# Kernel tuning notes

Measured on AMD Instinct MI355X. Metric: run time of the kernel, lower is better.

Reference implementation:

```python
import jax, jax.numpy as jnp
import numpy as np

S, B, CIN, COUT, H, W, K = 4, 32, 128, 256, 16, 16, 3
D = CIN * K * K  # 1152, patch feature size = in_features
PRIOR_PREC = 1.0  # isotropic prior precision (prior_prec_full = PRIOR_PREC * I_D)
LOG_PREC_LR = 1.0


def _patches(x, k):
    # x: [N, C, H, W] -> [N, C*k*k, H, W]; channel-major patch ordering (matches torch unfold)
    pad = k // 2
    return jax.lax.conv_general_dilated_patches(
        x, (k, k), (1, 1), ((pad, pad), (pad, pad)),
        dimension_numbers=('NCHW', 'OIHW', 'NCHW'))


def setup_inputs() -> dict:
    key = jax.random.key(0)
    k1, k2, k3, k4 = jax.random.split(key, 4)
    X = jax.random.normal(k1, (S, B, CIN, H, W), jnp.float32)
    u = jax.random.normal(k2, (B, COUT, H, W), jnp.float32)
    log_prec_scaled = jax.random.normal(k3, (B,), jnp.float32)
    Z = jax.random.normal(k4, (S, COUT, D), jnp.float32)  # standard normal noise for rsample
    return {"X": X, "u": u, "log_prec_scaled": log_prec_scaled, "Z": Z}


def reference(X, u, log_prec_scaled, Z):
    Xi = X[:, :B]  # [S, B, CIN, H, W]
    sqrt_prec = jnp.exp(0.5 * LOG_PREC_LR * log_prec_scaled)[:, None, None, None]  # [B,1,1,1]
    Xil = sqrt_prec * Xi                     # [S, B, CIN, H, W]
    Yil = sqrt_prec * u                      # [B, COUT, H, W]

    # conv_mm: sufficient statistics via patch extraction
    P = _patches(Xil.reshape(S * B, CIN, H, W), K).reshape(S, B, D, H * W)
    Yf = Yil.reshape(B, COUT, H * W)
    XLX = jnp.einsum('sbdp,sbep->sde', P, P)       # [S, D, D]
    XLY = jnp.einsum('sbdp,bcp->sdc', P, Yf)       # [S, D, COUT]

    # rsample_logpq_weights
    prec = XLX + PRIOR_PREC * jnp.eye(D, dtype=XLX.dtype)   # [S, D, D]
    L = jnp.linalg.cholesky(prec)                            # [S, D, D], lower
    logdet_prec = 2.0 * jnp.sum(jnp.log(jnp.diagonal(L, axis1=-2, axis2=-1)), -1)  # [S]

    mu = jax.scipy.linalg.cho_solve((L, True), XLY)          # [S, D, COUT]
    # dW: solve L^T dW = Z (multi-RHS; L is shared across COUT)
    dW = jax.scipy.linalg.solve_triangular(L, jnp.swapaxes(Z, -1, -2), lower=True, trans='T')
    Wm = jnp.swapaxes(mu + dW, -1, -2)                       # [S, COUT, D]

    # logP: unnormalized MVN log-prob of each output neuron's weights under N(0, PRIOR_PREC^-1 I)
    logP = (0.5 * COUT * D * jnp.log(jnp.asarray(PRIOR_PREC, Wm.dtype))
            - 0.5 * PRIOR_PREC * jnp.sum(Wm * Wm, (-1, -2)))          # [S]
    logQ = -0.5 * jnp.sum(Z * Z, (-1, -2)) + 0.5 * COUT * logdet_prec  # [S]
    logpq = logP - logQ
    return Wm, logpq
```

## Files before the change

### kernel.cpp

```cpp
#include <hip/hip_runtime.h>
#include <math.h>

#define NS 4
#define NB 32
#define CIN 128
#define NCOUT 256
#define HWN 256
#define ND 1152
#define NK 8192
static const size_t D2 = (size_t)ND * ND;

typedef __attribute__((ext_vector_type(8))) short bf16x8;
typedef __attribute__((ext_vector_type(4))) float f32x4;

static __device__ inline unsigned short f2bf(float x) {
  unsigned int u = __float_as_uint(x);
  unsigned int r = (u + 0x7fffu + ((u >> 16) & 1u)) >> 16;
  return (unsigned short)r;
}
static __device__ inline float bf2f(unsigned short h) {
  return __uint_as_float(((unsigned int)h) << 16);
}
static __device__ inline float rdlane(float v, int l) {
  return __int_as_float(__builtin_amdgcn_readlane(__float_as_int(v), l));
}
static __device__ __forceinline__ void waitflag(const int* f) {
  while (__hip_atomic_load(f, __ATOMIC_RELAXED, __HIP_MEMORY_SCOPE_AGENT) == 0)
    __builtin_amdgcn_s_sleep(1);
  (void)__hip_atomic_load(f, __ATOMIC_ACQUIRE, __HIP_MEMORY_SCOPE_AGENT);
}


__global__ void k_sqrtp(const float* __restrict__ lp, float* __restrict__ sp,
                        float* __restrict__ pp) {
  int b = threadIdx.x;
  if (b < NB) sp[b] = expf(0.5f * lp[b]);
  if (b < 8) pp[b] = 0.f;
}

__global__ __launch_bounds__(128) void k_patches(const float* __restrict__ X,
                                                 const float* __restrict__ sp,
                                                 unsigned short* __restrict__ Phi,
                                                 unsigned short* __restrict__ Plo) {
  int d = blockIdx.x, s = blockIdx.y, t = threadIdx.x;
  int c = d / 9, r = d % 9, ky = r / 3, kx = r % 3;
  int p0 = t * 2;
  int yy = (p0 >> 4) + ky - 1;
  int xx0 = (p0 & 15) + kx - 1;
  bool oky = (yy >= 0 && yy < 16);
  bool ok0 = oky && (xx0 >= 0) && (xx0 < 16);
  bool ok1 = oky && (xx0 + 1 >= 0) && (xx0 + 1 < 16);
  int xo = yy * 16 + xx0;
  size_t base = ((size_t)s * ND + d) * NK + p0;
  for (int b = 0; b < NB; ++b) {
    float sb = sp[b];
    const float* xb = X + ((size_t)(s * NB + b) * CIN + c) * HWN;
    float v0 = ok0 ? xb[xo] * sb : 0.f;
    float v1 = ok1 ? xb[xo + 1] * sb : 0.f;
    unsigned short h0 = f2bf(v0), h1 = f2bf(v1);
    unsigned short l0 = f2bf(v0 - bf2f(h0)), l1 = f2bf(v1 - bf2f(h1));
    size_t idx = base + (size_t)b * HWN;
    *(unsigned int*)(Phi + idx) = (unsigned int)h0 | ((unsigned int)h1 << 16);
    *(unsigned int*)(Plo + idx) = (unsigned int)l0 | ((unsigned int)l1 << 16);
  }
}

__global__ __launch_bounds__(128) void k_ytt(const float* __restrict__ u,
                                             const float* __restrict__ sp,
                                             unsigned short* __restrict__ Yhi,
                                             unsigned short* __restrict__ Ylo) {
  int c = blockIdx.x, t = threadIdx.x;
  int p0 = t * 2;
  for (int b = 0; b < NB; ++b) {
    float sb = sp[b];
    const float* ub = u + ((size_t)b * NCOUT + c) * HWN + p0;
    float v0 = ub[0] * sb, v1 = ub[1] * sb;
    unsigned short h0 = f2bf(v0), h1 = f2bf(v1);
    unsigned short l0 = f2bf(v0 - bf2f(h0)), l1 = f2bf(v1 - bf2f(h1));
    size_t idx = (size_t)c * NK + (size_t)b * HWN + p0;
    *(unsigned int*)(Yhi + idx) = (unsigned int)h0 | ((unsigned int)h1 << 16);
    *(unsigned int*)(Ylo + idx) = (unsigned int)l0 | ((unsigned int)l1 << 16);
  }
}

__global__ __launch_bounds__(256) void k_gemm_mfma(
    const unsigned short* __restrict__ Phi, const unsigned short* __restrict__ Plo,
    const unsigned short* __restrict__ Yhi, const unsigned short* __restrict__ Ylo,
    float* __restrict__ prec, float* __restrict__ prec2,
    float* __restrict__ XLY, float* __restrict__ XLY2) {
  int jt = blockIdx.x, it = blockIdx.y;
  int s = blockIdx.z >> 1, kp = blockIdx.z & 1;
  bool isX = (jt <= it);
  if (!isX && jt < 9) return;
  int i0 = it * 128;
  int j0;
  const unsigned short *Bh, *Bl;
  if (isX) {
    j0 = jt * 128;
    Bh = Phi + ((size_t)s * ND + j0) * NK;
    Bl = Plo + ((size_t)s * ND + j0) * NK;
  } else {
    j0 = (jt - 9) * 128;
    Bh = Yhi + (size_t)j0 * NK;
    Bl = Ylo + (size_t)j0 * NK;
  }
  const unsigned short* Ah = Phi + ((size_t)s * ND + i0) * NK;
  const unsigned short* Al = Plo + ((size_t)s * ND + i0) * NK;

  __shared__ unsigned short sAh[4096], sAl[4096], sBh[4096], sBl[4096];
  int tid = threadIdx.x, wave = tid >> 6, lane = tid & 63;
  int wr = wave >> 1, wc = wave & 1;

  f32x4 zero = {0.f, 0.f, 0.f, 0.f};
  f32x4 acc[4][4];
#pragma unroll
  for (int m = 0; m < 4; ++m)
#pragma unroll
    for (int n = 0; n < 4; ++n) acc[m][n] = zero;

  const unsigned short* srcs[4] = {Ah, Al, Bh, Bl};
  unsigned short* dsts[4] = {sAh, sAl, sBh, sBl};
  int r0l = lane >> 2;
  int ke = (lane & 3) * 8;
  int arow0 = wr * 64 + (lane & 15);
  int brow0 = wc * 64 + (lane & 15);
  int koff = (lane >> 4) * 8;

  int kbeg = kp * (NK / 2), kend = kbeg + NK / 2;
  for (int k0 = kbeg; k0 < kend; k0 += 32) {
    __syncthreads();
#pragma unroll
    for (int f = 0; f < 4; ++f) {
#pragma unroll
      for (int cc = 0; cc < 2; ++cc) {
        int c = wave * 2 + cc;
        const unsigned short* g = srcs[f] + (size_t)(c * 16 + r0l) * NK + k0 + ke;
        unsigned short* l = dsts[f] + c * 512;
        __builtin_amdgcn_global_load_lds(
            (const __attribute__((address_space(1))) void*)g,
            (__attribute__((address_space(3))) void*)l, 16, 0, 0);
      }
    }
    __syncthreads();
    bf16x8 ah[4], al[4], bh[4], bl[4];
#pragma unroll
    for (int m = 0; m < 4; ++m) {
      int off = (arow0 + m * 16) * 32 + koff;
      ah[m] = *(const bf16x8*)&sAh[off];
      al[m] = *(const bf16x8*)&sAl[off];
    }
#pragma unroll
    for (int n = 0; n < 4; ++n) {
      int off = (brow0 + n * 16) * 32 + koff;
      bh[n] = *(const bf16x8*)&sBh[off];
      bl[n] = *(const bf16x8*)&sBl[off];
    }
#pragma unroll
    for (int m = 0; m < 4; ++m)
#pragma unroll
      for (int n = 0; n < 4; ++n) {
        acc[m][n] = __builtin_amdgcn_mfma_f32_16x16x32_bf16(ah[m], bh[n], acc[m][n], 0, 0, 0);
        acc[m][n] = __builtin_amdgcn_mfma_f32_16x16x32_bf16(ah[m], bl[n], acc[m][n], 0, 0, 0);
        acc[m][n] = __builtin_amdgcn_mfma_f32_16x16x32_bf16(al[m], bh[n], acc[m][n], 0, 0, 0);
      }
  }

  if (isX) {
    float* base = (kp ? prec2 : prec) + (size_t)s * D2;
#pragma unroll
    for (int m = 0; m < 4; ++m) {
      int row = i0 + wr * 64 + m * 16 + (lane >> 4) * 4;
#pragma unroll
      for (int n = 0; n < 4; ++n) {
        int col = j0 + wc * 64 + n * 16 + (lane & 15);
        float* cp = base + (size_t)row * ND + col;
#pragma unroll
        for (int r = 0; r < 4; ++r) cp[(size_t)r * ND] = acc[m][n][r];
      }
    }
  } else {
    float* base = (kp ? XLY2 : XLY) + (size_t)s * ND * NCOUT;
#pragma unroll
    for (int m = 0; m < 4; ++m) {
      int row = i0 + wr * 64 + m * 16 + (lane >> 4) * 4;
#pragma unroll
      for (int n = 0; n < 4; ++n) {
        int col = j0 + wc * 64 + n * 16 + (lane & 15);
        float* cp = base + (size_t)row * NCOUT + col;
#pragma unroll
        for (int r = 0; r < 4; ++r) cp[(size_t)r * NCOUT] = acc[m][n][r];
      }
    }
  }
}


static __device__ __forceinline__ void factor64(
    float acc[4][4], float (&At)[64][68], float (&Bt)[64][68],
    int tid, int lane, int w, int tx, int ty,
    float* iA64q, float* logdq, int* flagq) {
  __syncthreads();
#pragma unroll
  for (int r = 0; r < 4; ++r)
#pragma unroll
    for (int e = 0; e < 4; ++e) At[ty * 4 + r][tx * 4 + e] = acc[r][e];
  {
    int rr = tid >> 2, cb2 = (tid & 3) * 16;
#pragma unroll
    for (int m = 0; m < 16; ++m) Bt[rr][cb2 + m] = (rr == cb2 + m) ? 1.f : 0.f;
  }
  __syncthreads();
  float diagv = 1.f;
  for (int p = 0; p < 8; ++p) {
    int c0 = p * 8;
    if (w == 0) {
      float pa[8], xb[8];
#pragma unroll
      for (int e = 0; e < 8; ++e) {
        pa[e] = At[lane][c0 + e];
        xb[e] = Bt[c0 + e][lane];
      }
#pragma unroll
      for (int j = 0; j < 8; ++j) {
        float dj = rdlane(pa[j], c0 + j);
        float r0 = __builtin_amdgcn_rsqf(dj);
        r0 = r0 * (1.5f - 0.5f * dj * r0 * r0);
        pa[j] *= r0;
        float xj = xb[j] * r0;
        xb[j] = xj;
        if (lane == c0 + j) diagv = dj * r0;
#pragma unroll
        for (int e = j + 1; e < 8; ++e) {
          float sv = rdlane(pa[j], c0 + e);
          pa[e] = fmaf(-pa[j], sv, pa[e]);
          xb[e] = fmaf(-sv, xj, xb[e]);
        }
      }
#pragma unroll
      for (int e = 0; e < 8; ++e) {
        At[lane][c0 + e] = pa[e];
        Bt[c0 + e][lane] = xb[e];
      }
    }
    __syncthreads();
    if (p < 7) {
      float La[8], Xp[8];
#pragma unroll
      for (int e = 0; e < 8; ++e) {
        La[e] = At[lane][c0 + e];
        Xp[e] = Bt[c0 + e][lane];
      }
      for (int c = c0 + 8 + w; c < 64; c += 4) {
        float Lc[8];
#pragma unroll
        for (int e = 0; e < 8; ++e) Lc[e] = At[c][c0 + e];
        float v = At[lane][c], vb = Bt[c][lane];
#pragma unroll
        for (int e = 0; e < 8; ++e) {
          v = fmaf(-La[e], Lc[e], v);
          vb = fmaf(-Lc[e], Xp[e], vb);
        }
        At[lane][c] = v;
        Bt[c][lane] = vb;
      }
      __syncthreads();
    }
  }
  if (w == 0) logdq[lane] = logf(diagv);
  {
    float* q = iA64q;
    int rr = tid >> 2, cb2 = (tid & 3) * 16;
#pragma unroll
    for (int m = 0; m < 4; ++m)
      *(float4*)(q + rr * 64 + cb2 + m * 4) = *(const float4*)&Bt[rr][cb2 + m * 4];
  }
  __threadfence();
  __syncthreads();
  if (tid == 0)
    __hip_atomic_store(flagq, 1, __ATOMIC_RELEASE, __HIP_MEMORY_SCOPE_AGENT);
}

__global__ __launch_bounds__(256, 3) void k_chol_dag(
    float* __restrict__ L, const float* __restrict__ Lp2,
    float* __restrict__ iA64, float* __restrict__ logd,
    int* __restrict__ flags) {
  int t0 = blockIdx.x, s = blockIdx.y;
  int bi = 0;
  while ((bi + 1) * (bi + 2) / 2 <= t0) ++bi;
  int bj = t0 - bi * (bi + 1) / 2;
  int ib = bi * 64, jb = bj * 64;
  float* Ls = L + (size_t)s * D2;
  const float* Ps = Lp2 + (size_t)s * D2;
  int* fc = flags + s * 324;
  int* pd = flags + 1584 + s * 18;

  __shared__ float At[64][68];
  __shared__ float Bt[64][68];
  int tid = threadIdx.x, tx = tid & 15, ty = tid >> 4;
  int lane = tid & 63, w = tid >> 6;

  float acc[4][4];
#pragma unroll
  for (int r = 0; r < 4; ++r) {
    size_t idx = (size_t)(ib + ty * 4 + r) * ND + jb + tx * 4;
    float4 v = *(const float4*)(Ls + idx);
    float4 v2 = *(const float4*)(Ps + idx);
    acc[r][0] = v.x + v2.x; acc[r][1] = v.y + v2.y;
    acc[r][2] = v.z + v2.z; acc[r][3] = v.w + v2.w;
  }
  if (bi == bj) {
#pragma unroll
    for (int r = 0; r < 4; ++r)
#pragma unroll
      for (int e = 0; e < 4; ++e)
        if (ty * 4 + r == tx * 4 + e) acc[r][e] += 1.f;
  }

  int kend_t = (bi == bj) ? (bi > 0 ? bi - 1 : 0) : bj;
  for (int k = 0; k < kend_t; ++k) {
    waitflag(&fc[bi * 18 + k]);
    waitflag(&fc[bj * 18 + k]);
    int kb = k * 64;
    {
      int a2 = tid >> 2, km = (tid & 3) * 4;
#pragma unroll
      for (int m = 0; m < 4; ++m) {
        float4 v = *(const float4*)(Ls + (size_t)(ib + a2) * ND + kb + km + m * 16);
        At[km + m * 16 + 0][a2] = v.x;
        At[km + m * 16 + 1][a2] = v.y;
        At[km + m * 16 + 2][a2] = v.z;
        At[km + m * 16 + 3][a2] = v.w;
        float4 u4 = *(const float4*)(Ls + (size_t)(jb + a2) * ND + kb + km + m * 16);
        Bt[km + m * 16 + 0][a2] = u4.x;
        Bt[km + m * 16 + 1][a2] = u4.y;
        Bt[km + m * 16 + 2][a2] = u4.z;
        Bt[km + m * 16 + 3][a2] = u4.w;
      }
    }
    __syncthreads();
#pragma unroll
    for (int kc = 0; kc < 64; ++kc) {
      float4 a4 = *(const float4*)&At[kc][ty * 4];
      float4 b4 = *(const float4*)&Bt[kc][tx * 4];
      float ar[4] = {a4.x, a4.y, a4.z, a4.w};
      float br[4] = {b4.x, b4.y, b4.z, b4.w};
#pragma unroll
      for (int r = 0; r < 4; ++r)
#pragma unroll
        for (int e = 0; e < 4; ++e) acc[r][e] = fmaf(-ar[r], br[e], acc[r][e]);
    }
    __syncthreads();
  }

  if (bi == bj) {
    if (bi == 0) {
      factor64(acc, At, Bt, tid, lane, w, tx, ty,
               iA64 + (size_t)(s * 18) * 4096, logd + (size_t)s * ND, &fc[0]);
    } else {
#pragma unroll
      for (int r = 0; r < 4; ++r) {
        float4 v = {acc[r][0], acc[r][1], acc[r][2], acc[r][3]};
        *(float4*)(Ls + (size_t)(ib + ty * 4 + r) * ND + ib + tx * 4) = v;
      }
      __threadfence();
      __syncthreads();
      if (tid == 0)
        __hip_atomic_store(&pd[bi], 1, __ATOMIC_RELEASE,
                           __HIP_MEMORY_SCOPE_AGENT);
    }
  } else {
#pragma unroll
    for (int r = 0; r < 4; ++r)
#pragma unroll
      for (int e = 0; e < 4; ++e) At[tx * 4 + e][ty * 4 + r] = acc[r][e];
    waitflag(&fc[bj * 18 + bj]);
    {
      const float* q = iA64 + (size_t)(s * 18 + bj) * 4096;
      int a2 = tid >> 2, km = (tid & 3) * 4;
#pragma unroll
      for (int m = 0; m < 4; ++m) {
        float4 v = *(const float4*)(q + a2 * 64 + km + m * 16);
        Bt[km + m * 16 + 0][a2] = v.x;
        Bt[km + m * 16 + 1][a2] = v.y;
        Bt[km + m * 16 + 2][a2] = v.z;
        Bt[km + m * 16 + 3][a2] = v.w;
      }
    }
    __syncthreads();
    float acc2[4][4] = {};
#pragma unroll
    for (int kc = 0; kc < 64; ++kc) {
      float4 a4 = *(const float4*)&At[kc][ty * 4];
      float4 b4 = *(const float4*)&Bt[kc][tx * 4];
      float ar[4] = {a4.x, a4.y, a4.z, a4.w};
      float br[4] = {b4.x, b4.y, b4.z, b4.w};
#pragma unroll
      for (int r = 0; r < 4; ++r)
#pragma unroll
        for (int e = 0; e < 4; ++e) acc2[r][e] = fmaf(ar[r], br[e], acc2[r][e]);
    }
#pragma unroll
    for (int r = 0; r < 4; ++r) {
      float4 v = {acc2[r][0], acc2[r][1], acc2[r][2], acc2[r][3]};
      *(float4*)(Ls + (size_t)(ib + ty * 4 + r) * ND + jb + tx * 4) = v;
    }
    __threadfence();
    __syncthreads();
    if (tid == 0)
      __hip_atomic_store(&fc[bi * 18 + bj], 1, __ATOMIC_RELEASE,
                         __HIP_MEMORY_SCOPE_AGENT);

    if (bj == bi - 1) {
#pragma unroll
      for (int r = 0; r < 4; ++r)
#pragma unroll
        for (int e = 0; e < 4; ++e) At[tx * 4 + e][ty * 4 + r] = acc2[r][e];
      waitflag(&pd[bi]);
#pragma unroll
      for (int r = 0; r < 4; ++r) {
        float4 v = *(const float4*)(Ls + (size_t)(ib + ty * 4 + r) * ND + ib + tx * 4);
        acc[r][0] = v.x; acc[r][1] = v.y; acc[r][2] = v.z; acc[r][3] = v.w;
      }
      __syncthreads();
#pragma unroll
      for (int kc = 0; kc < 64; ++kc) {
        float4 a4 = *(const float4*)&At[kc][ty * 4];
        float4 b4 = *(const float4*)&At[kc][tx * 4];
        float ar[4] = {a4.x, a4.y, a4.z, a4.w};
        float br[4] = {b4.x, b4.y, b4.z, b4.w};
#pragma unroll
        for (int r = 0; r < 4; ++r)
#pragma unroll
          for (int e = 0; e < 4; ++e) acc[r][e] = fmaf(-ar[r], br[e], acc[r][e]);
      }
      factor64(acc, At, Bt, tid, lane, w, tx, ty,
               iA64 + (size_t)(s * 18 + bi) * 4096, logd + (size_t)s * ND + ib,
               &fc[bi * 18 + bi]);
    }
  }
}

__global__ __launch_bounds__(256) void k_invd128(const float* __restrict__ L,
                                                 const float* __restrict__ iA64,
                                                 float* __restrict__ iD) {
  int q = blockIdx.x, s = blockIdx.y;
  int tid = threadIdx.x;
  const float* Ls = L + (size_t)s * D2;
  float* out = iD + ((size_t)(s * 9 + q)) * 16384;
  int b0 = q * 128;
  __shared__ float inv0[64][68];
  __shared__ float invCt[64][68];
  __shared__ float Bt[64][68];
  __shared__ float Tl[64][68];

  {
    const float* iA0 = iA64 + (size_t)(s * 18 + 2 * q) * 4096;
    const float* iA1 = iA0 + 4096;
    int i = tid >> 2, c4 = (tid & 3) * 16;
#pragma unroll
    for (int m = 0; m < 4; ++m) {
      float4 v0 = *(const float4*)(iA0 + i * 64 + c4 + m * 4);
      *(float4*)&inv0[i][c4 + m * 4] = v0;
      float4 v1 = *(const float4*)(iA1 + i * 64 + c4 + m * 4);
      invCt[c4 + m * 4 + 0][i] = v1.x;
      invCt[c4 + m * 4 + 1][i] = v1.y;
      invCt[c4 + m * 4 + 2][i] = v1.z;
      invCt[c4 + m * 4 + 3][i] = v1.w;
    }
    const float* src = Ls + (size_t)(b0 + 64 + i) * ND + b0 + c4;
#pragma unroll
    for (int m = 0; m < 4; ++m) {
      float4 v = *(const float4*)(src + m * 4);
      Bt[c4 + m * 4 + 0][i] = v.x;
      Bt[c4 + m * 4 + 1][i] = v.y;
      Bt[c4 + m * 4 + 2][i] = v.z;
      Bt[c4 + m * 4 + 3][i] = v.w;
    }
  }
  __syncthreads();

  int tx = tid & 15, ty = tid >> 4;
  float acc[4][4] = {};
#pragma unroll
  for (int k = 0; k < 64; ++k) {
    float a4[4], b4[4];
#pragma unroll
    for (int e = 0; e < 4; ++e) { a4[e] = Bt[k][ty * 4 + e]; b4[e] = inv0[k][tx * 4 + e]; }
#pragma unroll
    for (int r = 0; r < 4; ++r)
#pragma unroll
      for (int e = 0; e < 4; ++e) acc[r][e] = fmaf(a4[r], b4[e], acc[r][e]);
  }
#pragma unroll
  for (int r = 0; r < 4; ++r)
#pragma unroll
    for (int e = 0; e < 4; ++e) Tl[ty * 4 + r][tx * 4 + e] = acc[r][e];
  __syncthreads();
  float acc2[4][4] = {};
#pragma unroll
  for (int k = 0; k < 64; ++k) {
    float a4[4], b4[4];
#pragma unroll
    for (int e = 0; e < 4; ++e) { a4[e] = invCt[k][ty * 4 + e]; b4[e] = Tl[k][tx * 4 + e]; }
#pragma unroll
    for (int r = 0; r < 4; ++r)
#pragma unroll
      for (int e = 0; e < 4; ++e) acc2[r][e] = fmaf(a4[r], b4[e], acc2[r][e]);
  }
  {
    int rrow = tid >> 2, cc = (tid & 3) * 32;
    float* o = out + rrow * 128 + cc;
    if (cc < 64) {
#pragma unroll
      for (int m = 0; m < 8; ++m) {
        float4 v = {inv0[rrow][cc + m * 4 + 0], inv0[rrow][cc + m * 4 + 1],
                    inv0[rrow][cc + m * 4 + 2], inv0[rrow][cc + m * 4 + 3]};
        *(float4*)(o + m * 4) = v;
      }
    } else {
      float4 z = {0.f, 0.f, 0.f, 0.f};
#pragma unroll
      for (int m = 0; m < 8; ++m) *(float4*)(o + m * 4) = z;
    }
  }
#pragma unroll
  for (int r = 0; r < 4; ++r) {
    float4 v = {-acc2[r][0], -acc2[r][1], -acc2[r][2], -acc2[r][3]};
    *(float4*)(out + (size_t)(64 + ty * 4 + r) * 128 + tx * 4) = v;
  }
  {
    int i = tid >> 2, jc = (tid & 3) * 16;
#pragma unroll
    for (int m = 0; m < 4; ++m) {
      float4 v = {invCt[jc + m * 4 + 0][i], invCt[jc + m * 4 + 1][i],
                  invCt[jc + m * 4 + 2][i], invCt[jc + m * 4 + 3][i]};
      *(float4*)(out + (size_t)(64 + i) * 128 + 64 + jc + m * 4) = v;
    }
  }
}

__global__ __launch_bounds__(256) void k_solve2(
    const float* __restrict__ L, const float* __restrict__ iD,
    const float* __restrict__ B1, const float* __restrict__ B2,
    const float* __restrict__ Z, float* __restrict__ Xf, float* __restrict__ Xb,
    float* __restrict__ Wm, float* __restrict__ pp, int* __restrict__ flags) {
  int r = blockIdx.x, ct = blockIdx.y, s = blockIdx.z;
  int rb = r * 128, cb = ct * 64;
  const float* Ls = L + (size_t)s * D2;
  const float* Dq = iD + ((size_t)(s * 9 + r)) * 16384;
  float* Xfs = Xf + (size_t)s * ND * NCOUT;
  float* Xbs = Xb + (size_t)s * ND * NCOUT;
  int fbf = 1296 + (s * 4 + ct) * 9;
  int fbb = 1440 + (s * 4 + ct) * 9;

  __shared__ float sA[32][132];
  __shared__ float sB[32][68];
  __shared__ float red[8];
  int tid = threadIdx.x, tx = tid & 15, ty = tid >> 4;
  int wave = tid >> 6, lane = tid & 63;

  float acc[8][4];
#pragma unroll
  for (int ii = 0; ii < 8; ++ii) {
    size_t idx = (size_t)s * ND * NCOUT + (size_t)(rb + ty * 8 + ii) * NCOUT + cb + tx * 4;
    float4 v = *(const float4*)(B1 + idx);
    float4 v2 = *(const float4*)(B2 + idx);
    acc[ii][0] = v.x + v2.x; acc[ii][1] = v.y + v2.y;
    acc[ii][2] = v.z + v2.z; acc[ii][3] = v.w + v2.w;
  }
  for (int q = 0; q < r; ++q) {
    waitflag(&flags[fbf + q]);
    int qb = q * 128;
    for (int kk = 0; kk < 4; ++kk) {
      __syncthreads();
      {
        int i = tid >> 1, kb = (tid & 1) * 16;
        const float* src = Ls + (size_t)(rb + i) * ND + qb + kk * 32 + kb;
#pragma unroll
        for (int m = 0; m < 4; ++m) {
          float4 v = *(const float4*)(src + m * 4);
          sA[kb + m * 4 + 0][i] = v.x;
          sA[kb + m * 4 + 1][i] = v.y;
          sA[kb + m * 4 + 2][i] = v.z;
          sA[kb + m * 4 + 3][i] = v.w;
        }
      }
      {
        int k = tid >> 3, jb2 = (tid & 7) * 8;
        const float* src = Xfs + (size_t)(qb + kk * 32 + k) * NCOUT + cb + jb2;
        float4 v0 = *(const float4*)src;
        float4 v1 = *(const float4*)(src + 4);
        *(float4*)&sB[k][jb2] = v0;
        *(float4*)&sB[k][jb2 + 4] = v1;
      }
      __syncthreads();
#pragma unroll
      for (int k = 0; k < 32; ++k) {
        float4 a0 = *(const float4*)&sA[k][ty * 8];
        float4 a1 = *(const float4*)&sA[k][ty * 8 + 4];
        float4 b0 = *(const float4*)&sB[k][tx * 4];
        float a[8] = {a0.x, a0.y, a0.z, a0.w, a1.x, a1.y, a1.z, a1.w};
        float b[4] = {b0.x, b0.y, b0.z, b0.w};
#pragma unroll
        for (int ii = 0; ii < 8; ++ii)
#pragma unroll
          for (int j = 0; j < 4; ++j) acc[ii][j] = fmaf(-a[ii], b[j], acc[ii][j]);
      }
    }
  }
  float acc2[8][4] = {};
  for (int kk = 0; kk < 4; ++kk) {
    __syncthreads();
    if ((ty >> 2) == kk) {
      int kloc = ty * 8 - kk * 32;
#pragma unroll
      for (int ii = 0; ii < 8; ++ii) {
        float4 v = {acc[ii][0], acc[ii][1], acc[ii][2], acc[ii][3]};
        *(float4*)&sB[kloc + ii][tx * 4] = v;
      }
    }
    {
      int i = tid >> 1, kb = (tid & 1) * 16;
      const float* src = Dq + (size_t)i * 128 + kk * 32 + kb;
#pragma unroll
      for (int m = 0; m < 4; ++m) {
        float4 v = *(const float4*)(src + m * 4);
        sA[kb + m * 4 + 0][i] = v.x;
        sA[kb + m * 4 + 1][i] = v.y;
        sA[kb + m * 4 + 2][i] = v.z;
        sA[kb + m * 4 + 3][i] = v.w;
      }
    }
    __syncthreads();
#pragma unroll
    for (int k = 0; k < 32; ++k) {
      float4 a0 = *(const float4*)&sA[k][ty * 8];
      float4 a1 = *(const float4*)&sA[k][ty * 8 + 4];
      float4 b0 = *(const float4*)&sB[k][tx * 4];
      float a[8] = {a0.x, a0.y, a0.z, a0.w, a1.x, a1.y, a1.z, a1.w};
      float b[4] = {b0.x, b0.y, b0.z, b0.w};
#pragma unroll
      for (int ii = 0; ii < 8; ++ii)
#pragma unroll
        for (int j = 0; j < 4; ++j) acc2[ii][j] = fmaf(a[ii], b[j], acc2[ii][j]);
    }
  }
#pragma unroll
  for (int ii = 0; ii < 8; ++ii) {
    float4 v = {acc2[ii][0], acc2[ii][1], acc2[ii][2], acc2[ii][3]};
    *(float4*)(Xfs + (size_t)(rb + ty * 8 + ii) * NCOUT + cb + tx * 4) = v;
  }
  __threadfence();
  __syncthreads();
  if (tid == 0)
    __hip_atomic_store(&flags[fbf + r], 1, __ATOMIC_RELEASE,
                       __HIP_MEMORY_SCOPE_AGENT);

#pragma unroll
  for (int ii = 0; ii < 8; ++ii)
#pragma unroll
    for (int j = 0; j < 4; ++j) acc[ii][j] = acc2[ii][j];

  float zp = 0.f;
  for (int kk = 0; kk < 4; ++kk) {
    __syncthreads();
    {
      int c = tid >> 2, d8 = (tid & 3) * 8;
      const float* src = Z + ((size_t)(s * NCOUT) + cb + c) * ND + rb + kk * 32 + d8;
      float4 v0 = *(const float4*)src;
      float4 v1 = *(const float4*)(src + 4);
      sA[d8 + 0][c] = v0.x; sA[d8 + 1][c] = v0.y; sA[d8 + 2][c] = v0.z; sA[d8 + 3][c] = v0.w;
      sA[d8 + 4][c] = v1.x; sA[d8 + 5][c] = v1.y; sA[d8 + 6][c] = v1.z; sA[d8 + 7][c] = v1.w;
      zp += v0.x * v0.x + v0.y * v0.y + v0.z * v0.z + v0.w * v0.w;
      zp += v1.x * v1.x + v1.y * v1.y + v1.z * v1.z + v1.w * v1.w;
    }
    __syncthreads();
    if ((ty >> 2) == kk) {
      int kloc = ty * 8 - kk * 32;
#pragma unroll
      for (int ii = 0; ii < 8; ++ii) {
        float4 v = *(const float4*)&sA[kloc + ii][tx * 4];
        acc[ii][0] += v.x; acc[ii][1] += v.y; acc[ii][2] += v.z; acc[ii][3] += v.w;
      }
    }
  }
#pragma unroll
  for (int m2 = 32; m2 >= 1; m2 >>= 1) zp += __shfl_xor(zp, m2, 64);
  if (lane == 0) red[wave] = zp;
  __syncthreads();
  if (tid == 0) atomicAdd(pp + s, red[0] + red[1] + red[2] + red[3]);

  for (int q = 8; q > r; --q) {
    waitflag(&flags[fbb + q]);
    int qb = q * 128;
    for (int kk = 0; kk < 4; ++kk) {
      __syncthreads();
      {
        int k = tid >> 3, ib2 = (tid & 7) * 16;
        const float* src = Ls + (size_t)(qb + kk * 32 + k) * ND + rb + ib2;
#pragma unroll
        for (int m = 0; m < 4; ++m)
          *(float4*)&sA[k][ib2 + m * 4] = *(const float4*)(src + m * 4);
      }
      {
        int k = tid >> 3, jb2 = (tid & 7) * 8;
        const float* src = Xbs + (size_t)(qb + kk * 32 + k) * NCOUT + cb + jb2;
        float4 v0 = *(const float4*)src;
        float4 v1 = *(const float4*)(src + 4);
        *(float4*)&sB[k][jb2] = v0;
        *(float4*)&sB[k][jb2 + 4] = v1;
      }
      __syncthreads();
#pragma unroll
      for (int k = 0; k < 32; ++k) {
        float4 a0 = *(const float4*)&sA[k][ty * 8];
        float4 a1 = *(const float4*)&sA[k][ty * 8 + 4];
        float4 b0 = *(const float4*)&sB[k][tx * 4];
        float a[8] = {a0.x, a0.y, a0.z, a0.w, a1.x, a1.y, a1.z, a1.w};
        float b[4] = {b0.x, b0.y, b0.z, b0.w};
#pragma unroll
        for (int ii = 0; ii < 8; ++ii)
#pragma unroll
          for (int j = 0; j < 4; ++j) acc[ii][j] = fmaf(-a[ii], b[j], acc[ii][j]);
      }
    }
  }
#pragma unroll
  for (int ii = 0; ii < 8; ++ii)
#pragma unroll
    for (int j = 0; j < 4; ++j) acc2[ii][j] = 0.f;
  for (int kk = 0; kk < 4; ++kk) {
    __syncthreads();
    if ((ty >> 2) == kk) {
      int kloc = ty * 8 - kk * 32;
#pragma unroll
      for (int ii = 0; ii < 8; ++ii) {
        float4 v = {acc[ii][0], acc[ii][1], acc[ii][2], acc[ii][3]};
        *(float4*)&sB[kloc + ii][tx * 4] = v;
      }
    }
    {
      int k = tid >> 3, ib2 = (tid & 7) * 16;
      const float* src = Dq + (size_t)(kk * 32 + k) * 128 + ib2;
#pragma unroll
      for (int m = 0; m < 4; ++m)
        *(float4*)&sA[k][ib2 + m * 4] = *(const float4*)(src + m * 4);
    }
    __syncthreads();
#pragma unroll
    for (int k = 0; k < 32; ++k) {
      float4 a0 = *(const float4*)&sA[k][ty * 8];
      float4 a1 = *(const float4*)&sA[k][ty * 8 + 4];
      float4 b0 = *(const float4*)&sB[k][tx * 4];
      float a[8] = {a0.x, a0.y, a0.z, a0.w, a1.x, a1.y, a1.z, a1.w};
      float b[4] = {b0.x, b0.y, b0.z, b0.w};
#pragma unroll
      for (int ii = 0; ii < 8; ++ii)
#pragma unroll
        for (int j = 0; j < 4; ++j) acc2[ii][j] = fmaf(a[ii], b[j], acc2[ii][j]);
    }
  }
#pragma unroll
  for (int ii = 0; ii < 8; ++ii) {
    float4 v = {acc2[ii][0], acc2[ii][1], acc2[ii][2], acc2[ii][3]};
    *(float4*)(Xbs + (size_t)(rb + ty * 8 + ii) * NCOUT + cb + tx * 4) = v;
  }
  __threadfence();
  __syncthreads();
  if (tid == 0)
    __hip_atomic_store(&flags[fbb + r], 1, __ATOMIC_RELEASE,
                       __HIP_MEMORY_SCOPE_AGENT);
  float wp = 0.f;
#pragma unroll
  for (int ii = 0; ii < 8; ++ii)
#pragma unroll
    for (int j = 0; j < 4; ++j) wp += acc2[ii][j] * acc2[ii][j];
#pragma unroll
  for (int m2 = 32; m2 >= 1; m2 >>= 1) wp += __shfl_xor(wp, m2, 64);
  __syncthreads();
  if (lane == 0) red[wave] = wp;
  __syncthreads();
  if (tid == 0) atomicAdd(pp + 4 + s, red[0] + red[1] + red[2] + red[3]);
  for (int kk = 0; kk < 4; ++kk) {
    __syncthreads();
    if ((ty >> 2) == kk) {
      int kloc = ty * 8 - kk * 32;
#pragma unroll
      for (int ii = 0; ii < 8; ++ii) {
        float4 v = {acc2[ii][0], acc2[ii][1], acc2[ii][2], acc2[ii][3]};
        *(float4*)&sB[kloc + ii][tx * 4] = v;
      }
    }
    __syncthreads();
    {
      int c = tid >> 2, d8 = (tid & 3) * 8;
      float t0 = sB[d8 + 0][c], t1 = sB[d8 + 1][c], t2 = sB[d8 + 2][c], t3 = sB[d8 + 3][c];
      float t4 = sB[d8 + 4][c], t5 = sB[d8 + 5][c], t6 = sB[d8 + 6][c], t7 = sB[d8 + 7][c];
      float* dst = Wm + ((size_t)(s * NCOUT) + cb + c) * ND + rb + kk * 32 + d8;
      float4 w0 = {t0, t1, t2, t3}, w1 = {t4, t5, t6, t7};
      *(float4*)dst = w0;
      *(float4*)(dst + 4) = w1;
    }
  }
}

__global__ __launch_bounds__(256) void k_finalize(const float* __restrict__ logd,
                                                  const float* __restrict__ pp,
                                                  float* __restrict__ out) {
  int s = blockIdx.x, tid = threadIdx.x;
  __shared__ float r0[256];
  float l = 0.f;
  for (int i = tid; i < ND; i += 256) l += logd[s * ND + i];
  r0[tid] = l;
  __syncthreads();
  for (int off = 128; off; off >>= 1) {
    if (tid < off) r0[tid] += r0[tid + off];
    __syncthreads();
  }
  if (tid == 0) {
    float logdet = 2.0f * r0[0];
    out[s] = 0.5f * (pp[s] - pp[4 + s]) - 128.0f * logdet;
  }
}

extern "C" void kernel_launch(void* const* d_in, const int* in_sizes, int n_in,
                              void* d_out, int out_size, void* d_ws, size_t ws_size,
                              hipStream_t stream) {
  const float* X = (const float*)d_in[0];
  const float* u = (const float*)d_in[1];
  const float* lp = (const float*)d_in[2];
  const float* Z = (const float*)d_in[3];
  float* out = (float*)d_out;

  float* ws = (float*)d_ws;
  float* sp    = ws;
  float* invd  = sp + 64;
  float* logd  = invd + (size_t)NS * ND;
  float* pp    = logd + (size_t)NS * ND;
  int*   flags = (int*)(pp + 64);
  float* iD    = (float*)(flags + 2048);
  float* iA64  = iD + (size_t)NS * 9 * 16384;
  float* Xf    = iA64 + (size_t)NS * 18 * 4096;
  float* Xb    = Xf + (size_t)NS * ND * NCOUT;
  float* prec  = Xb + (size_t)NS * ND * NCOUT;
  float* prec2 = prec + (size_t)NS * D2;
  float* XLY   = prec2 + (size_t)NS * D2;
  float* XLY2  = XLY + (size_t)NS * ND * NCOUT;
  unsigned short* Phi = (unsigned short*)(XLY2 + (size_t)NS * ND * NCOUT);
  unsigned short* Plo = Phi + (size_t)NS * ND * NK;
  unsigned short* Yhi = Plo + (size_t)NS * ND * NK;
  unsigned short* Ylo = Yhi + (size_t)NCOUT * NK;

  hipMemsetAsync(flags, 0, 2048 * sizeof(int), stream);
  k_sqrtp<<<1, 64, 0, stream>>>(lp, sp, pp);
  k_patches<<<dim3(ND, NS), 128, 0, stream>>>(X, sp, Phi, Plo);
  k_ytt<<<NCOUT, 128, 0, stream>>>(u, sp, Yhi, Ylo);
  k_gemm_mfma<<<dim3(11, 9, NS * 2), 256, 0, stream>>>(Phi, Plo, Yhi, Ylo, prec,
                                                       prec2, XLY, XLY2);
  k_chol_dag<<<dim3(171, NS), 256, 0, stream>>>(prec, prec2, iA64, logd, flags);
  k_invd128<<<dim3(9, NS), 256, 0, stream>>>(prec, iA64, iD);
  k_solve2<<<dim3(9, 4, NS), 256, 0, stream>>>(prec, iD, XLY, XLY2, Z, Xf, Xb,
                                               out, pp, flags);
  k_finalize<<<NS, 256, 0, stream>>>(logd, pp, out + (size_t)NS * NCOUT * ND);
}
```

Measured before the change: 1.502 ms.

## Move final diagonal update and factor into diagonal block via pre-solve buffer

In the dataflow Cholesky, the diagonal block now performs its own final rank-64 update and factorization. It takes the unsolved sub-diagonal panel, which the neighbouring block publishes early to a scratch buffer (reusing the iD region), and multiplies it by the previous block's inverse. Before, the sub-diagonal block had to finish its triangular solve and then do the diagonal update itself, so the critical path is shortened by letting the diagonal block start as soon as the unsolved panel is ready. The diagonal SYRK loop also loads only one tile, since both operands are the same panel. It adds redundant recomputation of the solved panel and relies on iD being free as scratch before k_invd128 overwrites it.

```diff
diff --git a/kernel.cpp b/kernel.cpp
--- a/kernel.cpp
+++ b/kernel.cpp
@@ -283,7 +283,7 @@
 __global__ __launch_bounds__(256, 3) void k_chol_dag(
     float* __restrict__ L, const float* __restrict__ Lp2,
     float* __restrict__ iA64, float* __restrict__ logd,
-    int* __restrict__ flags) {
+    int* __restrict__ flags, float* __restrict__ pcb) {
   int t0 = blockIdx.x, s = blockIdx.y;
   int bi = 0;
   while ((bi + 1) * (bi + 2) / 2 <= t0) ++bi;
@@ -292,7 +292,8 @@
   float* Ls = L + (size_t)s * D2;
   const float* Ps = Lp2 + (size_t)s * D2;
   int* fc = flags + s * 324;
-  int* pd = flags + 1584 + s * 18;
+  int* pc = flags + 1584 + s * 18;
+  float* pcs = pcb + (size_t)(s * 18) * 4096;
 
   __shared__ float At[64][68];
   __shared__ float Bt[64][68];
@@ -319,7 +320,7 @@
   int kend_t = (bi == bj) ? (bi > 0 ? bi - 1 : 0) : bj;
   for (int k = 0; k < kend_t; ++k) {
     waitflag(&fc[bi * 18 + k]);
-    waitflag(&fc[bj * 18 + k]);
+    if (bi != bj) waitflag(&fc[bj * 18 + k]);
     int kb = k * 64;
     {
       int a2 = tid >> 2, km = (tid & 3) * 4;
@@ -330,24 +331,40 @@
         At[km + m * 16 + 1][a2] = v.y;
         At[km + m * 16 + 2][a2] = v.z;
         At[km + m * 16 + 3][a2] = v.w;
-        float4 u4 = *(const float4*)(Ls + (size_t)(jb + a2) * ND + kb + km + m * 16);
-        Bt[km + m * 16 + 0][a2] = u4.x;
-        Bt[km + m * 16 + 1][a2] = u4.y;
-        Bt[km + m * 16 + 2][a2] = u4.z;
-        Bt[km + m * 16 + 3][a2] = u4.w;
-      }
-    }
-    __syncthreads();
-#pragma unroll
-    for (int kc = 0; kc < 64; ++kc) {
-      float4 a4 = *(const float4*)&At[kc][ty * 4];
-      float4 b4 = *(const float4*)&Bt[kc][tx * 4];
-      float ar[4] = {a4.x, a4.y, a4.z, a4.w};
-      float br[4] = {b4.x, b4.y, b4.z, b4.w};
-#pragma unroll
-      for (int r = 0; r < 4; ++r)
-#pragma unroll
-        for (int e = 0; e < 4; ++e) acc[r][e] = fmaf(-ar[r], br[e], acc[r][e]);
+        if (bi != bj) {
+          float4 u4 = *(const float4*)(Ls + (size_t)(jb + a2) * ND + kb + km + m * 16);
+          Bt[km + m * 16 + 0][a2] = u4.x;
+          Bt[km + m * 16 + 1][a2] = u4.y;
+          Bt[km + m * 16 + 2][a2] = u4.z;
+          Bt[km + m * 16 + 3][a2] = u4.w;
+        }
+      }
+    }
+    __syncthreads();
+    if (bi == bj) {
+#pragma unroll
+      for (int kc = 0; kc < 64; ++kc) {
+        float4 a4 = *(const float4*)&At[kc][ty * 4];
+        float4 b4 = *(const float4*)&At[kc][tx * 4];
+        float ar[4] = {a4.x, a4.y, a4.z, a4.w};
+        float br[4] = {b4.x, b4.y, b4.z, b4.w};
+#pragma unroll
+        for (int r = 0; r < 4; ++r)
+#pragma unroll
+          for (int e = 0; e < 4; ++e) acc[r][e] = fmaf(-ar[r], br[e], acc[r][e]);
+      }
+    } else {
+#pragma unroll
+      for (int kc = 0; kc < 64; ++kc) {
+        float4 a4 = *(const float4*)&At[kc][ty * 4];
+        float4 b4 = *(const float4*)&Bt[kc][tx * 4];
+        float ar[4] = {a4.x, a4.y, a4.z, a4.w};
+        float br[4] = {b4.x, b4.y, b4.z, b4.w};
+#pragma unroll
+        for (int r = 0; r < 4; ++r)
+#pragma unroll
+          for (int e = 0; e < 4; ++e) acc[r][e] = fmaf(-ar[r], br[e], acc[r][e]);
+      }
     }
     __syncthreads();
   }
@@ -357,18 +374,82 @@
       factor64(acc, At, Bt, tid, lane, w, tx, ty,
                iA64 + (size_t)(s * 18) * 4096, logd + (size_t)s * ND, &fc[0]);
     } else {
-#pragma unroll
-      for (int r = 0; r < 4; ++r) {
-        float4 v = {acc[r][0], acc[r][1], acc[r][2], acc[r][3]};
-        *(float4*)(Ls + (size_t)(ib + ty * 4 + r) * ND + ib + tx * 4) = v;
+      waitflag(&pc[bi]);
+      {
+        const float* q = pcs + (size_t)bi * 4096;
+        int a2 = tid >> 2, km = (tid & 3) * 4;
+#pragma unroll
+        for (int m = 0; m < 4; ++m) {
+          float4 v = *(const float4*)(q + a2 * 64 + km + m * 16);
+          At[km + m * 16 + 0][a2] = v.x;
+          At[km + m * 16 + 1][a2] = v.y;
+          At[km + m * 16 + 2][a2] = v.z;
+          At[km + m * 16 + 3][a2] = v.w;
+        }
+      }
+      waitflag(&fc[(bi - 1) * 18 + (bi - 1)]);
+      {
+        const float* q = iA64 + (size_t)(s * 18 + bi - 1) * 4096;
+        int a2 = tid >> 2, km = (tid & 3) * 4;
+#pragma unroll
+        for (int m = 0; m < 4; ++m) {
+          float4 v = *(const float4*)(q + a2 * 64 + km + m * 16);
+          Bt[km + m * 16 + 0][a2] = v.x;
+          Bt[km + m * 16 + 1][a2] = v.y;
+          Bt[km + m * 16 + 2][a2] = v.z;
+          Bt[km + m * 16 + 3][a2] = v.w;
+        }
+      }
+      __syncthreads();
+      float c2[4][4] = {};
+#pragma unroll
+      for (int kc = 0; kc < 64; ++kc) {
+        float4 a4 = *(const float4*)&At[kc][ty * 4];
+        float4 b4 = *(const float4*)&Bt[kc][tx * 4];
+        float ar[4] = {a4.x, a4.y, a4.z, a4.w};
+        float br[4] = {b4.x, b4.y, b4.z, b4.w};
+#pragma unroll
+        for (int r = 0; r < 4; ++r)
+#pragma unroll
+          for (int e = 0; e < 4; ++e) c2[r][e] = fmaf(ar[r], br[e], c2[r][e]);
+      }
+      __syncthreads();
+#pragma unroll
+      for (int r = 0; r < 4; ++r)
+#pragma unroll
+        for (int e = 0; e < 4; ++e) At[tx * 4 + e][ty * 4 + r] = c2[r][e];
+      __syncthreads();
+#pragma unroll
+      for (int kc = 0; kc < 64; ++kc) {
+        float4 a4 = *(const float4*)&At[kc][ty * 4];
+        float4 b4 = *(const float4*)&At[kc][tx * 4];
+        float ar[4] = {a4.x, a4.y, a4.z, a4.w};
+        float br[4] = {b4.x, b4.y, b4.z, b4.w};
+#pragma unroll
+        for (int r = 0; r < 4; ++r)
+#pragma unroll
+          for (int e = 0; e < 4; ++e) acc[r][e] = fmaf(-ar[r], br[e], acc[r][e]);
+      }
+      factor64(acc, At, Bt, tid, lane, w, tx, ty,
+               iA64 + (size_t)(s * 18 + bi) * 4096, logd + (size_t)s * ND + ib,
+               &fc[bi * 18 + bi]);
+    }
+  } else {
+    if (bj == bi - 1) {
+      {
+        float* q = pcs + (size_t)bi * 4096;
+#pragma unroll
+        for (int r = 0; r < 4; ++r) {
+          float4 v = {acc[r][0], acc[r][1], acc[r][2], acc[r][3]};
+          *(float4*)(q + (size_t)(ty * 4 + r) * 64 + tx * 4) = v;
+        }
       }
       __threadfence();
       __syncthreads();
       if (tid == 0)
-        __hip_atomic_store(&pd[bi], 1, __ATOMIC_RELEASE,
+        __hip_atomic_store(&pc[bi], 1, __ATOMIC_RELEASE,
                            __HIP_MEMORY_SCOPE_AGENT);
     }
-  } else {
 #pragma unroll
     for (int r = 0; r < 4; ++r)
 #pragma unroll
@@ -409,34 +490,6 @@
     if (tid == 0)
       __hip_atomic_store(&fc[bi * 18 + bj], 1, __ATOMIC_RELEASE,
                          __HIP_MEMORY_SCOPE_AGENT);
-
-    if (bj == bi - 1) {
-#pragma unroll
-      for (int r = 0; r < 4; ++r)
-#pragma unroll
-        for (int e = 0; e < 4; ++e) At[tx * 4 + e][ty * 4 + r] = acc2[r][e];
-      waitflag(&pd[bi]);
-#pragma unroll
-      for (int r = 0; r < 4; ++r) {
-        float4 v = *(const float4*)(Ls + (size_t)(ib + ty * 4 + r) * ND + ib + tx * 4);
-        acc[r][0] = v.x; acc[r][1] = v.y; acc[r][2] = v.z; acc[r][3] = v.w;
-      }
-      __syncthreads();
-#pragma unroll
-      for (int kc = 0; kc < 64; ++kc) {
-        float4 a4 = *(const float4*)&At[kc][ty * 4];
-        float4 b4 = *(const float4*)&At[kc][tx * 4];
-        float ar[4] = {a4.x, a4.y, a4.z, a4.w};
-        float br[4] = {b4.x, b4.y, b4.z, b4.w};
-#pragma unroll
-        for (int r = 0; r < 4; ++r)
-#pragma unroll
-          for (int e = 0; e < 4; ++e) acc[r][e] = fmaf(-ar[r], br[e], acc[r][e]);
-      }
-      factor64(acc, At, Bt, tid, lane, w, tx, ty,
-               iA64 + (size_t)(s * 18 + bi) * 4096, logd + (size_t)s * ND + ib,
-               &fc[bi * 18 + bi]);
-    }
   }
 }
 
@@ -857,7 +910,7 @@
   k_ytt<<<NCOUT, 128, 0, stream>>>(u, sp, Yhi, Ylo);
   k_gemm_mfma<<<dim3(11, 9, NS * 2), 256, 0, stream>>>(Phi, Plo, Yhi, Ylo, prec,
                                                        prec2, XLY, XLY2);
-  k_chol_dag<<<dim3(171, NS), 256, 0, stream>>>(prec, prec2, iA64, logd, flags);
+  k_chol_dag<<<dim3(171, NS), 256, 0, stream>>>(prec, prec2, iA64, logd, flags, iD);
   k_invd128<<<dim3(9, NS), 256, 0, stream>>>(prec, iA64, iD);
   k_solve2<<<dim3(9, 4, NS), 256, 0, stream>>>(prec, iD, XLY, XLY2, Z, Xf, Xb,
                                                out, pp, flags);
```

After: 1.466 ms. 1.02x faster.
